# Kernel tuning notes

Hardware: AMD Instinct MI355X
Metric: run time of the kernel (lower is better)

Reference implementation:

```python
import jax, jax.numpy as jnp
import numpy as np

N_NODES = 50000
N_EDGES = 800000
D = 128


def gcn_conv(x, src, dst, W, b, num_nodes):
    # PyG GCNConv: h = X W; add self-loops; symmetric deg^-1/2 normalization; scatter-add; + bias
    h = x @ W                                   # [N, F_out]
    ones = jnp.ones(src.shape[0], dtype=h.dtype)
    deg = jax.ops.segment_sum(ones, dst, num_segments=num_nodes)  # in-degree incl. self-loops
    dinv = jax.lax.rsqrt(jnp.maximum(deg, 1.0))  # deg >= 1 because of self-loops
    norm = dinv[src] * dinv[dst]                 # [E+N]
    msg = h[src] * norm[:, None]                 # gather + scale
    out = jax.ops.segment_sum(msg, dst, num_segments=num_nodes)
    return out + b


def setup_inputs() -> dict:
    key = jax.random.key(0)
    ks = jax.random.split(key, 6)
    x = jax.random.normal(ks[0], (N_NODES, D), dtype=jnp.float32)
    edge_index = jax.random.randint(ks[1], (2, N_EDGES), 0, N_NODES, dtype=jnp.int64)
    s = 1.0 / np.sqrt(D)
    W1 = jax.random.normal(ks[2], (D, D), dtype=jnp.float32) * s
    W2 = jax.random.normal(ks[3], (D, D), dtype=jnp.float32) * s
    Wg = jax.random.normal(ks[4], (2 * D, D), dtype=jnp.float32) * (1.0 / np.sqrt(2 * D))
    b1 = jnp.zeros((D,), jnp.float32)
    b2 = jnp.zeros((D,), jnp.float32)
    bg = jnp.zeros((D,), jnp.float32)
    return {"x": x, "edge_index": edge_index, "W1": W1, "b1": b1,
            "W2": W2, "b2": b2, "Wg": Wg, "bg": bg}


def reference(x, edge_index, W1, b1, W2, b2, Wg, bg):
    num_nodes = x.shape[0]
    x0 = jnp.clip(x, -100.0, 100.0)
    loop = jnp.arange(num_nodes, dtype=edge_index.dtype)
    src = jnp.concatenate([edge_index[0], loop])
    dst = jnp.concatenate([edge_index[1], loop])
    h = jax.nn.relu(gcn_conv(x0, src, dst, W1, b1, num_nodes))
    # F.dropout(p=0.3, training=False) -> identity at inference
    h = jax.nn.relu(gcn_conv(h, src, dst, W2, b2, num_nodes))
    h = h + x0  # residual (out_channels == in_channels)
    gate = jax.nn.sigmoid(jnp.concatenate([h, x0], axis=1) @ Wg + bg)
    return h * gate
```

## Files before the change

### kernel.cpp

```cpp
#include <hip/hip_runtime.h>
#include <hip/hip_bf16.h>

using short8 = __attribute__((ext_vector_type(8))) short;
using f32x4  = __attribute__((ext_vector_type(4))) float;

static constexpr int NN = 50000;
static constexpr int NE = 800000;
static constexpr int MPAD = 50048;
static constexpr int NB2 = 256;
static constexpr int BNODE = 196;
static constexpr int CAPB = 4096;
static constexpr int NCHB = 200;
static constexpr int CHB = NE / NCHB;

__device__ __forceinline__ float clip100(float v) { return fminf(fmaxf(v, -100.f), 100.f); }
__device__ __forceinline__ unsigned short f2b(float v) {
    __hip_bfloat16 h = __float2bfloat16(v);
    return *reinterpret_cast<unsigned short*>(&h);
}
__device__ __forceinline__ float blo(unsigned int u) { return __uint_as_float(u << 16); }
__device__ __forceinline__ float bhi(unsigned int u) { return __uint_as_float(u & 0xFFFF0000u); }
__device__ __forceinline__ float b2f(unsigned short u) {
    return __uint_as_float(((unsigned int)u) << 16);
}

__global__ __launch_bounds__(256) void k_front(const int* __restrict__ idx,
                                               int2* __restrict__ epair,
                                               int* __restrict__ gcur,
                                               const float* __restrict__ W1,
                                               const float* __restrict__ W2,
                                               const float* __restrict__ Wg,
                                               unsigned short* __restrict__ Wt1,
                                               unsigned short* __restrict__ Wt2,
                                               unsigned short* __restrict__ Wgt) {
    __shared__ int ls[CHB], ld[CHB];
    __shared__ int bcnt[NB2], bb[NB2], bofs[NB2];
    const int tid = threadIdx.x;
    if (blockIdx.x < NCHB) {
        const int beg = blockIdx.x * CHB;
        for (int i = tid; i < CHB; i += 256) {
            ls[i] = idx[beg + i];
            ld[i] = idx[NE + beg + i];
        }
        bcnt[tid] = 0;
        __syncthreads();
        for (int i = tid; i < CHB; i += 256) atomicAdd(&bcnt[ld[i] / BNODE], 1);
        __syncthreads();
        bb[tid] = atomicAdd(&gcur[tid], bcnt[tid]);
        bofs[tid] = 0;
        __syncthreads();
        for (int i = tid; i < CHB; i += 256) {
            const int d = ld[i];
            const int p = d / BNODE;
            const int pos = atomicAdd(&bofs[p], 1);
            epair[p * CAPB + bb[p] + pos] = make_int2(ls[i], d);
        }
    } else {
        const int i = (blockIdx.x - NCHB) * 256 + tid;
        if (i < 16384) {
            const int n = i >> 7, k = i & 127;
            Wt1[i] = f2b(W1[k * 128 + n]);
        } else if (i < 32768) {
            const int j = i - 16384;
            const int n = j >> 7, k = j & 127;
            Wt2[j] = f2b(W2[k * 128 + n]);
        } else {
            const int j = i - 32768;
            const int n = j >> 8, k = j & 255;
            Wgt[j] = f2b(Wg[k * 128 + n]);
        }
    }
}

__global__ __launch_bounds__(256) void k_mid(const int2* __restrict__ epair,
                                             const int* __restrict__ gcur,
                                             int* __restrict__ rowptr,
                                             float* __restrict__ dinv,
                                             int* __restrict__ esrc,
                                             const float* __restrict__ x,
                                             const unsigned short* __restrict__ Wt,
                                             unsigned short* __restrict__ Cb) {
    __shared__ alignas(16) char smem[CAPB * 2 * 4 + 3 * 256 * 4];
    const int tid = threadIdx.x;
    if (blockIdx.x < NB2) {
        int* ls   = (int*)smem;
        int* ld   = ls + CAPB;
        int* cntL = ld + CAPB;
        int* sc   = cntL + 256;
        int* cur  = sc + 256;
        const int t = tid;
        const int b = blockIdx.x;
        sc[t] = gcur[t];
        __syncthreads();
        for (int off = 1; off < 256; off <<= 1) {
            const int add = (t >= off) ? sc[t - off] : 0;
            __syncthreads();
            sc[t] += add;
            __syncthreads();
        }
        const int ne = gcur[b];
        const int base = sc[b] - ne;
        const int nb0 = b * BNODE;
        const int nn = min(NN - nb0, BNODE);
        if (b == 0 && t == 0) rowptr[NN] = NE;

        for (int i = t; i < ne; i += 256) {
            const int2 p = epair[b * CAPB + i];
            ls[i] = p.x;
            ld[i] = p.y - nb0;
        }
        cntL[t] = 0;
        __syncthreads();
        for (int i = t; i < ne; i += 256) atomicAdd(&cntL[ld[i]], 1);
        __syncthreads();
        sc[t] = cntL[t];
        __syncthreads();
        for (int off = 1; off < 256; off <<= 1) {
            const int add = (t >= off) ? sc[t - off] : 0;
            __syncthreads();
            sc[t] += add;
            __syncthreads();
        }
        const int excl = sc[t] - cntL[t];
        cur[t] = excl;
        if (t < nn) {
            rowptr[nb0 + t] = base + excl;
            dinv[nb0 + t] = rsqrtf(1.f + (float)cntL[t]);
        }
        __syncthreads();
        for (int i = t; i < ne; i += 256) {
            const int pos = base + atomicAdd(&cur[ld[i]], 1);
            esrc[pos] = ls[i];
        }
    } else {
        unsigned short* wl = (unsigned short*)smem;
#pragma unroll
        for (int j = tid; j < 2048; j += 256) {
            const int row = j >> 4, c8 = j & 15;
            *(short8*)(wl + row * 136 + c8 * 8) = *(const short8*)(Wt + row * 128 + c8 * 8);
        }
        __syncthreads();

        const int wv = tid >> 6;
        const int ln = tid & 63;
        const int l16 = ln & 15;
        const int qd = ln >> 4;
        const int rowb = (blockIdx.x - NB2) * 64 + wv * 16;
        const long arow = rowb + l16;
        const int kq = qd * 8;

        f32x4 acc[8];
#pragma unroll
        for (int i = 0; i < 8; ++i) acc[i] = (f32x4){0.f, 0.f, 0.f, 0.f};

#pragma unroll
        for (int kc = 0; kc < 4; ++kc) {
            short8 a = (short8){0, 0, 0, 0, 0, 0, 0, 0};
            if (arow < NN) {
                const float* fp = x + arow * 128 + kc * 32 + kq;
                const float4 f0 = *(const float4*)fp;
                const float4 f1 = *(const float4*)(fp + 4);
                a[0] = (short)f2b(clip100(f0.x));
                a[1] = (short)f2b(clip100(f0.y));
                a[2] = (short)f2b(clip100(f0.z));
                a[3] = (short)f2b(clip100(f0.w));
                a[4] = (short)f2b(clip100(f1.x));
                a[5] = (short)f2b(clip100(f1.y));
                a[6] = (short)f2b(clip100(f1.z));
                a[7] = (short)f2b(clip100(f1.w));
            }
#pragma unroll
            for (int nt = 0; nt < 8; ++nt) {
                const short8 b = *(const short8*)(wl + (nt * 16 + l16) * 136 + kc * 32 + kq);
                acc[nt] = __builtin_amdgcn_mfma_f32_16x16x32_bf16(a, b, acc[nt], 0, 0, 0);
            }
        }

        const int r0 = rowb + qd * 4;
#pragma unroll
        for (int r = 0; r < 4; ++r) {
            const int row = r0 + r;
            if (row < NN) {
#pragma unroll
                for (int nt = 0; nt < 8; ++nt) {
                    Cb[(long)row * 128 + nt * 16 + l16] = f2b(acc[nt][r]);
                }
            }
        }
    }
}

__global__ __launch_bounds__(256) void k_mfma2(const unsigned short* __restrict__ Ab,
                                               const unsigned short* __restrict__ Wt,
                                               unsigned short* __restrict__ Cb,
                                               const float* __restrict__ dinv) {
    __shared__ unsigned short wl[128 * 136];
    const int tid = threadIdx.x;
#pragma unroll
    for (int j = tid; j < 2048; j += 256) {
        const int row = j >> 4, c8 = j & 15;
        *(short8*)(wl + row * 136 + c8 * 8) = *(const short8*)(Wt + row * 128 + c8 * 8);
    }
    __syncthreads();

    const int wv = tid >> 6;
    const int ln = tid & 63;
    const int l16 = ln & 15;
    const int qd = ln >> 4;
    const int rowb = blockIdx.x * 64 + wv * 16;
    const long arow = rowb + l16;
    const int kq = qd * 8;

    f32x4 acc[8];
#pragma unroll
    for (int i = 0; i < 8; ++i) acc[i] = (f32x4){0.f, 0.f, 0.f, 0.f};

#pragma unroll
    for (int kc = 0; kc < 4; ++kc) {
        const short8 a = *(const short8*)(Ab + arow * 128 + kc * 32 + kq);
#pragma unroll
        for (int nt = 0; nt < 8; ++nt) {
            const short8 b = *(const short8*)(wl + (nt * 16 + l16) * 136 + kc * 32 + kq);
            acc[nt] = __builtin_amdgcn_mfma_f32_16x16x32_bf16(a, b, acc[nt], 0, 0, 0);
        }
    }

    const int r0 = rowb + qd * 4;
#pragma unroll
    for (int r = 0; r < 4; ++r) {
        const int row = r0 + r;
        if (row < NN) {
            const float dv = dinv[row];
#pragma unroll
            for (int nt = 0; nt < 8; ++nt) {
                Cb[(long)row * 128 + nt * 16 + l16] = f2b(acc[nt][r] * dv);
            }
        }
    }
}

__global__ __launch_bounds__(256) void k_mfma_gate(const unsigned short* __restrict__ Ab,
                                                   const float* __restrict__ Af,
                                                   const unsigned short* __restrict__ Wt,
                                                   const float* __restrict__ bg,
                                                   float* __restrict__ out) {
    __shared__ unsigned short wl[128 * 136];
    const int tid = threadIdx.x;
    const int wv = tid >> 6;
    const int ln = tid & 63;
    const int l16 = ln & 15;
    const int qd = ln >> 4;
    const int rowb = blockIdx.x * 64 + wv * 16;
    const long arow = rowb + l16;
    const int kq = qd * 8;

    f32x4 acc[8];
#pragma unroll
    for (int i = 0; i < 8; ++i) acc[i] = (f32x4){0.f, 0.f, 0.f, 0.f};

#pragma unroll
    for (int j = tid; j < 2048; j += 256) {
        const int row = j >> 4, c8 = j & 15;
        *(short8*)(wl + row * 136 + c8 * 8) = *(const short8*)(Wt + row * 256 + c8 * 8);
    }
    __syncthreads();
    {
        const unsigned short* ap = Ab + arow * 128 + kq;
#pragma unroll
        for (int kc = 0; kc < 4; ++kc) {
            const short8 a = *(const short8*)(ap + kc * 32);
#pragma unroll
            for (int nt = 0; nt < 8; ++nt) {
                const short8 b = *(const short8*)(wl + (nt * 16 + l16) * 136 + kc * 32 + kq);
                acc[nt] = __builtin_amdgcn_mfma_f32_16x16x32_bf16(a, b, acc[nt], 0, 0, 0);
            }
        }
    }
    __syncthreads();

#pragma unroll
    for (int j = tid; j < 2048; j += 256) {
        const int row = j >> 4, c8 = j & 15;
        *(short8*)(wl + row * 136 + c8 * 8) = *(const short8*)(Wt + row * 256 + 128 + c8 * 8);
    }
    __syncthreads();
    {
        const bool valid = arow < NN;
        const float* fp = Af + arow * 128 + kq;
#pragma unroll
        for (int kc = 0; kc < 4; ++kc) {
            short8 a = (short8){0, 0, 0, 0, 0, 0, 0, 0};
            if (valid) {
                const float4 f0 = *(const float4*)(fp + kc * 32);
                const float4 f1 = *(const float4*)(fp + kc * 32 + 4);
                a[0] = (short)f2b(clip100(f0.x));
                a[1] = (short)f2b(clip100(f0.y));
                a[2] = (short)f2b(clip100(f0.z));
                a[3] = (short)f2b(clip100(f0.w));
                a[4] = (short)f2b(clip100(f1.x));
                a[5] = (short)f2b(clip100(f1.y));
                a[6] = (short)f2b(clip100(f1.z));
                a[7] = (short)f2b(clip100(f1.w));
            }
#pragma unroll
            for (int nt = 0; nt < 8; ++nt) {
                const short8 b = *(const short8*)(wl + (nt * 16 + l16) * 136 + kc * 32 + kq);
                acc[nt] = __builtin_amdgcn_mfma_f32_16x16x32_bf16(a, b, acc[nt], 0, 0, 0);
            }
        }
    }

    const int r0 = rowb + qd * 4;
#pragma unroll
    for (int nt = 0; nt < 8; ++nt) {
        const int col = nt * 16 + l16;
        const float bgv = bg[col];
#pragma unroll
        for (int r = 0; r < 4; ++r) {
            const int row = r0 + r;
            if (row < NN) {
                const float g = 1.f / (1.f + __expf(-(acc[nt][r] + bgv)));
                const float ov = b2f(Ab[(long)row * 128 + col]) * g;
                __builtin_nontemporal_store(ov, &out[(long)row * 128 + col]);
            }
        }
    }
}

template <bool RES, bool ESCALE>
__global__ __launch_bounds__(256) void k_aggr(const unsigned int* __restrict__ As2,
                                              unsigned short* __restrict__ Bb,
                                              const int* __restrict__ rowptr,
                                              const int* __restrict__ esrc,
                                              const float* __restrict__ dinv,
                                              const float* __restrict__ bias,
                                              const float* __restrict__ x) {
    const int d = __builtin_amdgcn_readfirstlane((blockIdx.x * 256 + threadIdx.x) >> 6);
    if (d >= NN) return;
    const int lane = threadIdx.x & 63;
    const float dd = dinv[d];

    const unsigned int u = As2[(long)d * 64 + lane];
    float2 acc;
    if (ESCALE) {
        acc.x = blo(u) * dd;
        acc.y = bhi(u) * dd;
    } else {
        acc.x = blo(u);
        acc.y = bhi(u);
    }

    const int beg = rowptr[d];
    const int end = rowptr[d + 1];
    int i = beg;
    for (; i + 16 <= end; i += 16) {
        int s[16];
#pragma unroll
        for (int e = 0; e < 16; ++e) s[e] = esrc[i + e];
        unsigned int v[16];
#pragma unroll
        for (int e = 0; e < 16; ++e) v[e] = As2[(long)s[e] * 64 + lane];
        if (ESCALE) {
            float px = 0.f, py = 0.f;
#pragma unroll
            for (int e = 0; e < 16; ++e) {
                const float w = dinv[s[e]];
                px = fmaf(blo(v[e]), w, px);
                py = fmaf(bhi(v[e]), w, py);
            }
            acc.x += px;
            acc.y += py;
        } else {
            float px = 0.f, py = 0.f;
#pragma unroll
            for (int e = 0; e < 16; ++e) {
                px += blo(v[e]);
                py += bhi(v[e]);
            }
            acc.x += px;
            acc.y += py;
        }
    }
    if (i + 8 <= end) {
        const int s0 = esrc[i + 0], s1 = esrc[i + 1], s2 = esrc[i + 2], s3 = esrc[i + 3];
        const int s4 = esrc[i + 4], s5 = esrc[i + 5], s6 = esrc[i + 6], s7 = esrc[i + 7];
        const unsigned int v0 = As2[(long)s0 * 64 + lane];
        const unsigned int v1 = As2[(long)s1 * 64 + lane];
        const unsigned int v2 = As2[(long)s2 * 64 + lane];
        const unsigned int v3 = As2[(long)s3 * 64 + lane];
        const unsigned int v4 = As2[(long)s4 * 64 + lane];
        const unsigned int v5 = As2[(long)s5 * 64 + lane];
        const unsigned int v6 = As2[(long)s6 * 64 + lane];
        const unsigned int v7 = As2[(long)s7 * 64 + lane];
        if (ESCALE) {
            const float w0 = dinv[s0], w1 = dinv[s1], w2 = dinv[s2], w3 = dinv[s3];
            const float w4 = dinv[s4], w5 = dinv[s5], w6 = dinv[s6], w7 = dinv[s7];
            acc.x += ((blo(v0) * w0 + blo(v1) * w1) + (blo(v2) * w2 + blo(v3) * w3)) +
                     ((blo(v4) * w4 + blo(v5) * w5) + (blo(v6) * w6 + blo(v7) * w7));
            acc.y += ((bhi(v0) * w0 + bhi(v1) * w1) + (bhi(v2) * w2 + bhi(v3) * w3)) +
                     ((bhi(v4) * w4 + bhi(v5) * w5) + (bhi(v6) * w6 + bhi(v7) * w7));
        } else {
            acc.x += ((blo(v0) + blo(v1)) + (blo(v2) + blo(v3))) +
                     ((blo(v4) + blo(v5)) + (blo(v6) + blo(v7)));
            acc.y += ((bhi(v0) + bhi(v1)) + (bhi(v2) + bhi(v3))) +
                     ((bhi(v4) + bhi(v5)) + (bhi(v6) + bhi(v7)));
        }
        i += 8;
    }
    if (i + 4 <= end) {
        const int s0 = esrc[i + 0], s1 = esrc[i + 1], s2 = esrc[i + 2], s3 = esrc[i + 3];
        const unsigned int v0 = As2[(long)s0 * 64 + lane];
        const unsigned int v1 = As2[(long)s1 * 64 + lane];
        const unsigned int v2 = As2[(long)s2 * 64 + lane];
        const unsigned int v3 = As2[(long)s3 * 64 + lane];
        if (ESCALE) {
            const float w0 = dinv[s0], w1 = dinv[s1], w2 = dinv[s2], w3 = dinv[s3];
            acc.x += (blo(v0) * w0 + blo(v1) * w1) + (blo(v2) * w2 + blo(v3) * w3);
            acc.y += (bhi(v0) * w0 + bhi(v1) * w1) + (bhi(v2) * w2 + bhi(v3) * w3);
        } else {
            acc.x += (blo(v0) + blo(v1)) + (blo(v2) + blo(v3));
            acc.y += (bhi(v0) + bhi(v1)) + (bhi(v2) + bhi(v3));
        }
        i += 4;
    }
    for (; i < end; ++i) {
        const int s = esrc[i];
        const unsigned int v = As2[(long)s * 64 + lane];
        if (ESCALE) {
            const float w = dinv[s];
            acc.x = fmaf(blo(v), w, acc.x);
            acc.y = fmaf(bhi(v), w, acc.y);
        } else {
            acc.x += blo(v);
            acc.y += bhi(v);
        }
    }

    const float2 bv = ((const float2*)bias)[lane];
    acc.x = fmaxf(fmaf(acc.x, dd, bv.x), 0.f);
    acc.y = fmaxf(fmaf(acc.y, dd, bv.y), 0.f);
    if (RES) {
        const float2 xv = ((const float2*)x)[(long)d * 64 + lane];
        acc.x += clip100(xv.x);
        acc.y += clip100(xv.y);
    }
    const unsigned int pack = (unsigned int)f2b(acc.x) | ((unsigned int)f2b(acc.y) << 16);
    ((unsigned int*)Bb)[(long)d * 64 + lane] = pack;
}

extern "C" void kernel_launch(void* const* d_in, const int* in_sizes, int n_in,
                              void* d_out, int out_size, void* d_ws, size_t ws_size,
                              hipStream_t stream) {
    const float* x  = (const float*)d_in[0];
    const int*  eix = (const int*)d_in[1];
    const float* W1 = (const float*)d_in[2];
    const float* b1 = (const float*)d_in[3];
    const float* W2 = (const float*)d_in[4];
    const float* b2 = (const float*)d_in[5];
    const float* Wg = (const float*)d_in[6];
    const float* bg = (const float*)d_in[7];
    float* out = (float*)d_out;

    char* ws = (char*)d_ws;
    unsigned short* As   = (unsigned short*)ws;
    unsigned short* hb   = (unsigned short*)(ws + 12812288);
    unsigned short* Wt1  = (unsigned short*)(ws + 25624576);
    unsigned short* Wt2  = (unsigned short*)(ws + 25657344);
    unsigned short* Wgt  = (unsigned short*)(ws + 25690112);
    int*   rowptr = (int*)(ws + 25755648);
    float* dinv   = (float*)(ws + 25956352);
    int*   gcur   = (int*)(ws + 26157056);
    int*   esrc   = (int*)(ws + 26159104);
    int2*  epair  = (int2*)(ws + 29359104);

    const int ggrid = MPAD / 64;
    dim3 blk(256);

    hipMemsetAsync(gcur, 0, NB2 * sizeof(int), stream);

    k_front<<<NCHB + 256, blk, 0, stream>>>(eix, epair, gcur, W1, W2, Wg, Wt1, Wt2, Wgt);

    k_mid<<<NB2 + ggrid, blk, 0, stream>>>(epair, gcur, rowptr, dinv, esrc, x, Wt1, As);

    k_aggr<false, true><<<(NN * 64 + 255) / 256, blk, 0, stream>>>(
        (const unsigned int*)As, hb, rowptr, esrc, dinv, b1, nullptr);

    k_mfma2<<<ggrid, blk, 0, stream>>>(hb, Wt2, As, dinv);

    k_aggr<true, false><<<(NN * 64 + 255) / 256, blk, 0, stream>>>(
        (const unsigned int*)As, hb, rowptr, esrc, dinv, b2, x);

    k_mfma_gate<<<ggrid, blk, 0, stream>>>(hb, x, Wgt, bg, out);
}
```

Before: 212.0 us.

## Fuse neighbor aggregation with following MFMA GEMMs via shared-memory tiles

Replaces the separate aggregation kernels and the GEMM kernels with two fused kernels. Each wave aggregates 16 nodes sequentially into a shared-memory bf16 tile, then the block runs the MFMA product against the staged weights. This removes the global round trip of the intermediate hidden features and two launches. The cost is less parallelism in aggregation: one wave now serially handles 16 nodes in a grid of about 782 blocks, where before each node had its own wave, so latency hiding in the gather may suffer.

```diff
diff --git a/kernel.cpp b/kernel.cpp
--- a/kernel.cpp
+++ b/kernel.cpp
@@ -24,322 +24,15 @@
     return __uint_as_float(((unsigned int)u) << 16);
 }
 
-__global__ __launch_bounds__(256) void k_front(const int* __restrict__ idx,
-                                               int2* __restrict__ epair,
-                                               int* __restrict__ gcur,
-                                               const float* __restrict__ W1,
-                                               const float* __restrict__ W2,
-                                               const float* __restrict__ Wg,
-                                               unsigned short* __restrict__ Wt1,
-                                               unsigned short* __restrict__ Wt2,
-                                               unsigned short* __restrict__ Wgt) {
-    __shared__ int ls[CHB], ld[CHB];
-    __shared__ int bcnt[NB2], bb[NB2], bofs[NB2];
-    const int tid = threadIdx.x;
-    if (blockIdx.x < NCHB) {
-        const int beg = blockIdx.x * CHB;
-        for (int i = tid; i < CHB; i += 256) {
-            ls[i] = idx[beg + i];
-            ld[i] = idx[NE + beg + i];
-        }
-        bcnt[tid] = 0;
-        __syncthreads();
-        for (int i = tid; i < CHB; i += 256) atomicAdd(&bcnt[ld[i] / BNODE], 1);
-        __syncthreads();
-        bb[tid] = atomicAdd(&gcur[tid], bcnt[tid]);
-        bofs[tid] = 0;
-        __syncthreads();
-        for (int i = tid; i < CHB; i += 256) {
-            const int d = ld[i];
-            const int p = d / BNODE;
-            const int pos = atomicAdd(&bofs[p], 1);
-            epair[p * CAPB + bb[p] + pos] = make_int2(ls[i], d);
-        }
-    } else {
-        const int i = (blockIdx.x - NCHB) * 256 + tid;
-        if (i < 16384) {
-            const int n = i >> 7, k = i & 127;
-            Wt1[i] = f2b(W1[k * 128 + n]);
-        } else if (i < 32768) {
-            const int j = i - 16384;
-            const int n = j >> 7, k = j & 127;
-            Wt2[j] = f2b(W2[k * 128 + n]);
-        } else {
-            const int j = i - 32768;
-            const int n = j >> 8, k = j & 255;
-            Wgt[j] = f2b(Wg[k * 128 + n]);
-        }
-    }
-}
-
-__global__ __launch_bounds__(256) void k_mid(const int2* __restrict__ epair,
-                                             const int* __restrict__ gcur,
-                                             int* __restrict__ rowptr,
-                                             float* __restrict__ dinv,
-                                             int* __restrict__ esrc,
-                                             const float* __restrict__ x,
-                                             const unsigned short* __restrict__ Wt,
-                                             unsigned short* __restrict__ Cb) {
-    __shared__ alignas(16) char smem[CAPB * 2 * 4 + 3 * 256 * 4];
-    const int tid = threadIdx.x;
-    if (blockIdx.x < NB2) {
-        int* ls   = (int*)smem;
-        int* ld   = ls + CAPB;
-        int* cntL = ld + CAPB;
-        int* sc   = cntL + 256;
-        int* cur  = sc + 256;
-        const int t = tid;
-        const int b = blockIdx.x;
-        sc[t] = gcur[t];
-        __syncthreads();
-        for (int off = 1; off < 256; off <<= 1) {
-            const int add = (t >= off) ? sc[t - off] : 0;
-            __syncthreads();
-            sc[t] += add;
-            __syncthreads();
-        }
-        const int ne = gcur[b];
-        const int base = sc[b] - ne;
-        const int nb0 = b * BNODE;
-        const int nn = min(NN - nb0, BNODE);
-        if (b == 0 && t == 0) rowptr[NN] = NE;
-
-        for (int i = t; i < ne; i += 256) {
-            const int2 p = epair[b * CAPB + i];
-            ls[i] = p.x;
-            ld[i] = p.y - nb0;
-        }
-        cntL[t] = 0;
-        __syncthreads();
-        for (int i = t; i < ne; i += 256) atomicAdd(&cntL[ld[i]], 1);
-        __syncthreads();
-        sc[t] = cntL[t];
-        __syncthreads();
-        for (int off = 1; off < 256; off <<= 1) {
-            const int add = (t >= off) ? sc[t - off] : 0;
-            __syncthreads();
-            sc[t] += add;
-            __syncthreads();
-        }
-        const int excl = sc[t] - cntL[t];
-        cur[t] = excl;
-        if (t < nn) {
-            rowptr[nb0 + t] = base + excl;
-            dinv[nb0 + t] = rsqrtf(1.f + (float)cntL[t]);
-        }
-        __syncthreads();
-        for (int i = t; i < ne; i += 256) {
-            const int pos = base + atomicAdd(&cur[ld[i]], 1);
-            esrc[pos] = ls[i];
-        }
-    } else {
-        unsigned short* wl = (unsigned short*)smem;
-#pragma unroll
-        for (int j = tid; j < 2048; j += 256) {
-            const int row = j >> 4, c8 = j & 15;
-            *(short8*)(wl + row * 136 + c8 * 8) = *(const short8*)(Wt + row * 128 + c8 * 8);
-        }
-        __syncthreads();
-
-        const int wv = tid >> 6;
-        const int ln = tid & 63;
-        const int l16 = ln & 15;
-        const int qd = ln >> 4;
-        const int rowb = (blockIdx.x - NB2) * 64 + wv * 16;
-        const long arow = rowb + l16;
-        const int kq = qd * 8;
-
-        f32x4 acc[8];
-#pragma unroll
-        for (int i = 0; i < 8; ++i) acc[i] = (f32x4){0.f, 0.f, 0.f, 0.f};
-
-#pragma unroll
-        for (int kc = 0; kc < 4; ++kc) {
-            short8 a = (short8){0, 0, 0, 0, 0, 0, 0, 0};
-            if (arow < NN) {
-                const float* fp = x + arow * 128 + kc * 32 + kq;
-                const float4 f0 = *(const float4*)fp;
-                const float4 f1 = *(const float4*)(fp + 4);
-                a[0] = (short)f2b(clip100(f0.x));
-                a[1] = (short)f2b(clip100(f0.y));
-                a[2] = (short)f2b(clip100(f0.z));
-                a[3] = (short)f2b(clip100(f0.w));
-                a[4] = (short)f2b(clip100(f1.x));
-                a[5] = (short)f2b(clip100(f1.y));
-                a[6] = (short)f2b(clip100(f1.z));
-                a[7] = (short)f2b(clip100(f1.w));
-            }
-#pragma unroll
-            for (int nt = 0; nt < 8; ++nt) {
-                const short8 b = *(const short8*)(wl + (nt * 16 + l16) * 136 + kc * 32 + kq);
-                acc[nt] = __builtin_amdgcn_mfma_f32_16x16x32_bf16(a, b, acc[nt], 0, 0, 0);
-            }
-        }
-
-        const int r0 = rowb + qd * 4;
-#pragma unroll
-        for (int r = 0; r < 4; ++r) {
-            const int row = r0 + r;
-            if (row < NN) {
-#pragma unroll
-                for (int nt = 0; nt < 8; ++nt) {
-                    Cb[(long)row * 128 + nt * 16 + l16] = f2b(acc[nt][r]);
-                }
-            }
-        }
-    }
-}
-
-__global__ __launch_bounds__(256) void k_mfma2(const unsigned short* __restrict__ Ab,
-                                               const unsigned short* __restrict__ Wt,
-                                               unsigned short* __restrict__ Cb,
-                                               const float* __restrict__ dinv) {
-    __shared__ unsigned short wl[128 * 136];
-    const int tid = threadIdx.x;
-#pragma unroll
-    for (int j = tid; j < 2048; j += 256) {
-        const int row = j >> 4, c8 = j & 15;
-        *(short8*)(wl + row * 136 + c8 * 8) = *(const short8*)(Wt + row * 128 + c8 * 8);
-    }
-    __syncthreads();
-
-    const int wv = tid >> 6;
-    const int ln = tid & 63;
-    const int l16 = ln & 15;
-    const int qd = ln >> 4;
-    const int rowb = blockIdx.x * 64 + wv * 16;
-    const long arow = rowb + l16;
-    const int kq = qd * 8;
-
-    f32x4 acc[8];
-#pragma unroll
-    for (int i = 0; i < 8; ++i) acc[i] = (f32x4){0.f, 0.f, 0.f, 0.f};
-
-#pragma unroll
-    for (int kc = 0; kc < 4; ++kc) {
-        const short8 a = *(const short8*)(Ab + arow * 128 + kc * 32 + kq);
-#pragma unroll
-        for (int nt = 0; nt < 8; ++nt) {
-            const short8 b = *(const short8*)(wl + (nt * 16 + l16) * 136 + kc * 32 + kq);
-            acc[nt] = __builtin_amdgcn_mfma_f32_16x16x32_bf16(a, b, acc[nt], 0, 0, 0);
-        }
-    }
-
-    const int r0 = rowb + qd * 4;
-#pragma unroll
-    for (int r = 0; r < 4; ++r) {
-        const int row = r0 + r;
-        if (row < NN) {
-            const float dv = dinv[row];
-#pragma unroll
-            for (int nt = 0; nt < 8; ++nt) {
-                Cb[(long)row * 128 + nt * 16 + l16] = f2b(acc[nt][r] * dv);
-            }
-        }
-    }
-}
-
-__global__ __launch_bounds__(256) void k_mfma_gate(const unsigned short* __restrict__ Ab,
-                                                   const float* __restrict__ Af,
-                                                   const unsigned short* __restrict__ Wt,
-                                                   const float* __restrict__ bg,
-                                                   float* __restrict__ out) {
-    __shared__ unsigned short wl[128 * 136];
-    const int tid = threadIdx.x;
-    const int wv = tid >> 6;
-    const int ln = tid & 63;
-    const int l16 = ln & 15;
-    const int qd = ln >> 4;
-    const int rowb = blockIdx.x * 64 + wv * 16;
-    const long arow = rowb + l16;
-    const int kq = qd * 8;
-
-    f32x4 acc[8];
-#pragma unroll
-    for (int i = 0; i < 8; ++i) acc[i] = (f32x4){0.f, 0.f, 0.f, 0.f};
-
-#pragma unroll
-    for (int j = tid; j < 2048; j += 256) {
-        const int row = j >> 4, c8 = j & 15;
-        *(short8*)(wl + row * 136 + c8 * 8) = *(const short8*)(Wt + row * 256 + c8 * 8);
-    }
-    __syncthreads();
-    {
-        const unsigned short* ap = Ab + arow * 128 + kq;
-#pragma unroll
-        for (int kc = 0; kc < 4; ++kc) {
-            const short8 a = *(const short8*)(ap + kc * 32);
-#pragma unroll
-            for (int nt = 0; nt < 8; ++nt) {
-                const short8 b = *(const short8*)(wl + (nt * 16 + l16) * 136 + kc * 32 + kq);
-                acc[nt] = __builtin_amdgcn_mfma_f32_16x16x32_bf16(a, b, acc[nt], 0, 0, 0);
-            }
-        }
-    }
-    __syncthreads();
-
-#pragma unroll
-    for (int j = tid; j < 2048; j += 256) {
-        const int row = j >> 4, c8 = j & 15;
-        *(short8*)(wl + row * 136 + c8 * 8) = *(const short8*)(Wt + row * 256 + 128 + c8 * 8);
-    }
-    __syncthreads();
-    {
-        const bool valid = arow < NN;
-        const float* fp = Af + arow * 128 + kq;
-#pragma unroll
-        for (int kc = 0; kc < 4; ++kc) {
-            short8 a = (short8){0, 0, 0, 0, 0, 0, 0, 0};
-            if (valid) {
-                const float4 f0 = *(const float4*)(fp + kc * 32);
-                const float4 f1 = *(const float4*)(fp + kc * 32 + 4);
-                a[0] = (short)f2b(clip100(f0.x));
-                a[1] = (short)f2b(clip100(f0.y));
-                a[2] = (short)f2b(clip100(f0.z));
-                a[3] = (short)f2b(clip100(f0.w));
-                a[4] = (short)f2b(clip100(f1.x));
-                a[5] = (short)f2b(clip100(f1.y));
-                a[6] = (short)f2b(clip100(f1.z));
-                a[7] = (short)f2b(clip100(f1.w));
-            }
-#pragma unroll
-            for (int nt = 0; nt < 8; ++nt) {
-                const short8 b = *(const short8*)(wl + (nt * 16 + l16) * 136 + kc * 32 + kq);
-                acc[nt] = __builtin_amdgcn_mfma_f32_16x16x32_bf16(a, b, acc[nt], 0, 0, 0);
-            }
-        }
-    }
-
-    const int r0 = rowb + qd * 4;
-#pragma unroll
-    for (int nt = 0; nt < 8; ++nt) {
-        const int col = nt * 16 + l16;
-        const float bgv = bg[col];
-#pragma unroll
-        for (int r = 0; r < 4; ++r) {
-            const int row = r0 + r;
-            if (row < NN) {
-                const float g = 1.f / (1.f + __expf(-(acc[nt][r] + bgv)));
-                const float ov = b2f(Ab[(long)row * 128 + col]) * g;
-                __builtin_nontemporal_store(ov, &out[(long)row * 128 + col]);
-            }
-        }
-    }
-}
-
 template <bool RES, bool ESCALE>
-__global__ __launch_bounds__(256) void k_aggr(const unsigned int* __restrict__ As2,
-                                              unsigned short* __restrict__ Bb,
-                                              const int* __restrict__ rowptr,
-                                              const int* __restrict__ esrc,
-                                              const float* __restrict__ dinv,
-                                              const float* __restrict__ bias,
-                                              const float* __restrict__ x) {
-    const int d = __builtin_amdgcn_readfirstlane((blockIdx.x * 256 + threadIdx.x) >> 6);
-    if (d >= NN) return;
-    const int lane = threadIdx.x & 63;
+__device__ __forceinline__ unsigned int aggr_node(const int d, const int lane,
+                                                  const unsigned int* __restrict__ As2,
+                                                  const int* __restrict__ rowptr,
+                                                  const int* __restrict__ esrc,
+                                                  const float* __restrict__ dinv,
+                                                  const float* __restrict__ bias,
+                                                  const float* __restrict__ x) {
     const float dd = dinv[d];
-
     const unsigned int u = As2[(long)d * 64 + lane];
     float2 acc;
     if (ESCALE) {
@@ -349,7 +42,6 @@
         acc.x = blo(u);
         acc.y = bhi(u);
     }
-
     const int beg = rowptr[d];
     const int end = rowptr[d + 1];
     int i = beg;
@@ -360,26 +52,23 @@
         unsigned int v[16];
 #pragma unroll
         for (int e = 0; e < 16; ++e) v[e] = As2[(long)s[e] * 64 + lane];
+        float px = 0.f, py = 0.f;
         if (ESCALE) {
-            float px = 0.f, py = 0.f;
 #pragma unroll
             for (int e = 0; e < 16; ++e) {
                 const float w = dinv[s[e]];
                 px = fmaf(blo(v[e]), w, px);
                 py = fmaf(bhi(v[e]), w, py);
             }
-            acc.x += px;
-            acc.y += py;
         } else {
-            float px = 0.f, py = 0.f;
 #pragma unroll
             for (int e = 0; e < 16; ++e) {
                 px += blo(v[e]);
                 py += bhi(v[e]);
             }
-            acc.x += px;
-            acc.y += py;
-        }
+        }
+        acc.x += px;
+        acc.y += py;
     }
     if (i + 8 <= end) {
         const int s0 = esrc[i + 0], s1 = esrc[i + 1], s2 = esrc[i + 2], s3 = esrc[i + 3];
@@ -435,7 +124,6 @@
             acc.y += bhi(v);
         }
     }
-
     const float2 bv = ((const float2*)bias)[lane];
     acc.x = fmaxf(fmaf(acc.x, dd, bv.x), 0.f);
     acc.y = fmaxf(fmaf(acc.y, dd, bv.y), 0.f);
@@ -444,8 +132,332 @@
         acc.x += clip100(xv.x);
         acc.y += clip100(xv.y);
     }
-    const unsigned int pack = (unsigned int)f2b(acc.x) | ((unsigned int)f2b(acc.y) << 16);
-    ((unsigned int*)Bb)[(long)d * 64 + lane] = pack;
+    return (unsigned int)f2b(acc.x) | ((unsigned int)f2b(acc.y) << 16);
+}
+
+__global__ __launch_bounds__(256) void k_front(const int* __restrict__ idx,
+                                               int2* __restrict__ epair,
+                                               int* __restrict__ gcur,
+                                               const float* __restrict__ W1,
+                                               const float* __restrict__ W2,
+                                               const float* __restrict__ Wg,
+                                               unsigned short* __restrict__ Wt1,
+                                               unsigned short* __restrict__ Wt2,
+                                               unsigned short* __restrict__ Wgt) {
+    __shared__ int ls[CHB], ld[CHB];
+    __shared__ int bcnt[NB2], bb[NB2], bofs[NB2];
+    const int tid = threadIdx.x;
+    if (blockIdx.x < NCHB) {
+        const int beg = blockIdx.x * CHB;
+        for (int i = tid; i < CHB; i += 256) {
+            ls[i] = idx[beg + i];
+            ld[i] = idx[NE + beg + i];
+        }
+        bcnt[tid] = 0;
+        __syncthreads();
+        for (int i = tid; i < CHB; i += 256) atomicAdd(&bcnt[ld[i] / BNODE], 1);
+        __syncthreads();
+        bb[tid] = atomicAdd(&gcur[tid], bcnt[tid]);
+        bofs[tid] = 0;
+        __syncthreads();
+        for (int i = tid; i < CHB; i += 256) {
+            const int d = ld[i];
+            const int p = d / BNODE;
+            const int pos = atomicAdd(&bofs[p], 1);
+            epair[p * CAPB + bb[p] + pos] = make_int2(ls[i], d);
+        }
+    } else {
+        const int i = (blockIdx.x - NCHB) * 256 + tid;
+        if (i < 16384) {
+            const int n = i >> 7, k = i & 127;
+            Wt1[i] = f2b(W1[k * 128 + n]);
+        } else if (i < 32768) {
+            const int j = i - 16384;
+            const int n = j >> 7, k = j & 127;
+            Wt2[j] = f2b(W2[k * 128 + n]);
+        } else {
+            const int j = i - 32768;
+            const int n = j >> 8, k = j & 255;
+            Wgt[j] = f2b(Wg[k * 128 + n]);
+        }
+    }
+}
+
+__global__ __launch_bounds__(256) void k_mid(const int2* __restrict__ epair,
+                                             const int* __restrict__ gcur,
+                                             int* __restrict__ rowptr,
+                                             float* __restrict__ dinv,
+                                             int* __restrict__ esrc,
+                                             const float* __restrict__ x,
+                                             const unsigned short* __restrict__ Wt,
+                                             unsigned short* __restrict__ Cb) {
+    __shared__ alignas(16) char smem[CAPB * 2 * 4 + 3 * 256 * 4];
+    const int tid = threadIdx.x;
+    if (blockIdx.x < NB2) {
+        int* ls   = (int*)smem;
+        int* ld   = ls + CAPB;
+        int* cntL = ld + CAPB;
+        int* sc   = cntL + 256;
+        int* cur  = sc + 256;
+        const int t = tid;
+        const int b = blockIdx.x;
+        sc[t] = gcur[t];
+        __syncthreads();
+        for (int off = 1; off < 256; off <<= 1) {
+            const int add = (t >= off) ? sc[t - off] : 0;
+            __syncthreads();
+            sc[t] += add;
+            __syncthreads();
+        }
+        const int ne = gcur[b];
+        const int base = sc[b] - ne;
+        const int nb0 = b * BNODE;
+        const int nn = min(NN - nb0, BNODE);
+        if (b == 0 && t == 0) rowptr[NN] = NE;
+
+        for (int i = t; i < ne; i += 256) {
+            const int2 p = epair[b * CAPB + i];
+            ls[i] = p.x;
+            ld[i] = p.y - nb0;
+        }
+        cntL[t] = 0;
+        __syncthreads();
+        for (int i = t; i < ne; i += 256) atomicAdd(&cntL[ld[i]], 1);
+        __syncthreads();
+        sc[t] = cntL[t];
+        __syncthreads();
+        for (int off = 1; off < 256; off <<= 1) {
+            const int add = (t >= off) ? sc[t - off] : 0;
+            __syncthreads();
+            sc[t] += add;
+            __syncthreads();
+        }
+        const int excl = sc[t] - cntL[t];
+        cur[t] = excl;
+        if (t < nn) {
+            rowptr[nb0 + t] = base + excl;
+            dinv[nb0 + t] = rsqrtf(1.f + (float)cntL[t]);
+        }
+        __syncthreads();
+        for (int i = t; i < ne; i += 256) {
+            const int pos = base + atomicAdd(&cur[ld[i]], 1);
+            esrc[pos] = ls[i];
+        }
+    } else {
+        unsigned short* wl = (unsigned short*)smem;
+#pragma unroll
+        for (int j = tid; j < 2048; j += 256) {
+            const int row = j >> 4, c8 = j & 15;
+            *(short8*)(wl + row * 136 + c8 * 8) = *(const short8*)(Wt + row * 128 + c8 * 8);
+        }
+        __syncthreads();
+
+        const int wv = tid >> 6;
+        const int ln = tid & 63;
+        const int l16 = ln & 15;
+        const int qd = ln >> 4;
+        const int rowb = (blockIdx.x - NB2) * 64 + wv * 16;
+        const long arow = rowb + l16;
+        const int kq = qd * 8;
+
+        f32x4 acc[8];
+#pragma unroll
+        for (int i = 0; i < 8; ++i) acc[i] = (f32x4){0.f, 0.f, 0.f, 0.f};
+
+#pragma unroll
+        for (int kc = 0; kc < 4; ++kc) {
+            short8 a = (short8){0, 0, 0, 0, 0, 0, 0, 0};
+            if (arow < NN) {
+                const float* fp = x + arow * 128 + kc * 32 + kq;
+                const float4 f0 = *(const float4*)fp;
+                const float4 f1 = *(const float4*)(fp + 4);
+                a[0] = (short)f2b(clip100(f0.x));
+                a[1] = (short)f2b(clip100(f0.y));
+                a[2] = (short)f2b(clip100(f0.z));
+                a[3] = (short)f2b(clip100(f0.w));
+                a[4] = (short)f2b(clip100(f1.x));
+                a[5] = (short)f2b(clip100(f1.y));
+                a[6] = (short)f2b(clip100(f1.z));
+                a[7] = (short)f2b(clip100(f1.w));
+            }
+#pragma unroll
+            for (int nt = 0; nt < 8; ++nt) {
+                const short8 b = *(const short8*)(wl + (nt * 16 + l16) * 136 + kc * 32 + kq);
+                acc[nt] = __builtin_amdgcn_mfma_f32_16x16x32_bf16(a, b, acc[nt], 0, 0, 0);
+            }
+        }
+
+        const int r0 = rowb + qd * 4;
+#pragma unroll
+        for (int r = 0; r < 4; ++r) {
+            const int row = r0 + r;
+            if (row < NN) {
+#pragma unroll
+                for (int nt = 0; nt < 8; ++nt) {
+                    Cb[(long)row * 128 + nt * 16 + l16] = f2b(acc[nt][r]);
+                }
+            }
+        }
+    }
+}
+
+__global__ __launch_bounds__(256) void k_ag1(const unsigned int* __restrict__ As2,
+                                             const unsigned short* __restrict__ Wt2,
+                                             unsigned short* __restrict__ Cb,
+                                             const int* __restrict__ rowptr,
+                                             const int* __restrict__ esrc,
+                                             const float* __restrict__ dinv,
+                                             const float* __restrict__ b1) {
+    __shared__ alignas(16) unsigned int ht[64 * 68];
+    __shared__ unsigned short wl[128 * 136];
+    const int tid = threadIdx.x;
+#pragma unroll
+    for (int j = tid; j < 2048; j += 256) {
+        const int row = j >> 4, c8 = j & 15;
+        *(short8*)(wl + row * 136 + c8 * 8) = *(const short8*)(Wt2 + row * 128 + c8 * 8);
+    }
+    const int wv = tid >> 6;
+    const int ln = tid & 63;
+    const int nbase = blockIdx.x * 64 + wv * 16;
+#pragma unroll 1
+    for (int j = 0; j < 16; ++j) {
+        const int d = __builtin_amdgcn_readfirstlane(nbase + j);
+        unsigned int pack = 0;
+        if (d < NN)
+            pack = aggr_node<false, true>(d, ln, As2, rowptr, esrc, dinv, b1, nullptr);
+        ht[(wv * 16 + j) * 68 + ln] = pack;
+    }
+    __syncthreads();
+
+    const int l16 = ln & 15;
+    const int qd = ln >> 4;
+    const int kq = qd * 8;
+    f32x4 acc[8];
+#pragma unroll
+    for (int i = 0; i < 8; ++i) acc[i] = (f32x4){0.f, 0.f, 0.f, 0.f};
+#pragma unroll
+    for (int kc = 0; kc < 4; ++kc) {
+        const short8 a =
+            *(const short8*)((const unsigned short*)ht + (wv * 16 + l16) * 136 + kc * 32 + kq);
+#pragma unroll
+        for (int nt = 0; nt < 8; ++nt) {
+            const short8 b = *(const short8*)(wl + (nt * 16 + l16) * 136 + kc * 32 + kq);
+            acc[nt] = __builtin_amdgcn_mfma_f32_16x16x32_bf16(a, b, acc[nt], 0, 0, 0);
+        }
+    }
+    const int r0 = blockIdx.x * 64 + wv * 16 + qd * 4;
+#pragma unroll
+    for (int r = 0; r < 4; ++r) {
+        const int row = r0 + r;
+        if (row < NN) {
+            const float dv = dinv[row];
+#pragma unroll
+            for (int nt = 0; nt < 8; ++nt) {
+                Cb[(long)row * 128 + nt * 16 + l16] = f2b(acc[nt][r] * dv);
+            }
+        }
+    }
+}
+
+__global__ __launch_bounds__(256) void k_ag2(const unsigned int* __restrict__ Hs2,
+                                             const float* __restrict__ x,
+                                             const unsigned short* __restrict__ Wgt,
+                                             const int* __restrict__ rowptr,
+                                             const int* __restrict__ esrc,
+                                             const float* __restrict__ dinv,
+                                             const float* __restrict__ b2,
+                                             const float* __restrict__ bg,
+                                             float* __restrict__ out) {
+    __shared__ alignas(16) unsigned int ht[64 * 68];
+    __shared__ unsigned short wl[128 * 136];
+    const int tid = threadIdx.x;
+#pragma unroll
+    for (int j = tid; j < 2048; j += 256) {
+        const int row = j >> 4, c8 = j & 15;
+        *(short8*)(wl + row * 136 + c8 * 8) = *(const short8*)(Wgt + row * 256 + c8 * 8);
+    }
+    const int wv = tid >> 6;
+    const int ln = tid & 63;
+    const int nbase = blockIdx.x * 64 + wv * 16;
+#pragma unroll 1
+    for (int j = 0; j < 16; ++j) {
+        const int d = __builtin_amdgcn_readfirstlane(nbase + j);
+        unsigned int pack = 0;
+        if (d < NN)
+            pack = aggr_node<true, false>(d, ln, Hs2, rowptr, esrc, dinv, b2, x);
+        ht[(wv * 16 + j) * 68 + ln] = pack;
+    }
+    __syncthreads();
+
+    const int l16 = ln & 15;
+    const int qd = ln >> 4;
+    const int kq = qd * 8;
+    f32x4 acc[8];
+#pragma unroll
+    for (int i = 0; i < 8; ++i) acc[i] = (f32x4){0.f, 0.f, 0.f, 0.f};
+
+#pragma unroll
+    for (int kc = 0; kc < 4; ++kc) {
+        const short8 a =
+            *(const short8*)((const unsigned short*)ht + (wv * 16 + l16) * 136 + kc * 32 + kq);
+#pragma unroll
+        for (int nt = 0; nt < 8; ++nt) {
+            const short8 b = *(const short8*)(wl + (nt * 16 + l16) * 136 + kc * 32 + kq);
+            acc[nt] = __builtin_amdgcn_mfma_f32_16x16x32_bf16(a, b, acc[nt], 0, 0, 0);
+        }
+    }
+    __syncthreads();
+
+#pragma unroll
+    for (int j = tid; j < 2048; j += 256) {
+        const int row = j >> 4, c8 = j & 15;
+        *(short8*)(wl + row * 136 + c8 * 8) = *(const short8*)(Wgt + row * 256 + 128 + c8 * 8);
+    }
+    __syncthreads();
+
+    {
+        const long arow = (long)blockIdx.x * 64 + wv * 16 + l16;
+        const bool valid = arow < NN;
+        const float* fp = x + arow * 128 + kq;
+#pragma unroll
+        for (int kc = 0; kc < 4; ++kc) {
+            short8 a = (short8){0, 0, 0, 0, 0, 0, 0, 0};
+            if (valid) {
+                const float4 f0 = *(const float4*)(fp + kc * 32);
+                const float4 f1 = *(const float4*)(fp + kc * 32 + 4);
+                a[0] = (short)f2b(clip100(f0.x));
+                a[1] = (short)f2b(clip100(f0.y));
+                a[2] = (short)f2b(clip100(f0.z));
+                a[3] = (short)f2b(clip100(f0.w));
+                a[4] = (short)f2b(clip100(f1.x));
+                a[5] = (short)f2b(clip100(f1.y));
+                a[6] = (short)f2b(clip100(f1.z));
+                a[7] = (short)f2b(clip100(f1.w));
+            }
+#pragma unroll
+            for (int nt = 0; nt < 8; ++nt) {
+                const short8 b = *(const short8*)(wl + (nt * 16 + l16) * 136 + kc * 32 + kq);
+                acc[nt] = __builtin_amdgcn_mfma_f32_16x16x32_bf16(a, b, acc[nt], 0, 0, 0);
+            }
+        }
+    }
+
+    const int r0 = blockIdx.x * 64 + wv * 16 + qd * 4;
+#pragma unroll
+    for (int nt = 0; nt < 8; ++nt) {
+        const int col = nt * 16 + l16;
+        const float bgv = bg[col];
+#pragma unroll
+        for (int r = 0; r < 4; ++r) {
+            const int row = r0 + r;
+            if (row < NN) {
+                const float g = 1.f / (1.f + __expf(-(acc[nt][r] + bgv)));
+                const unsigned int hu = ht[(wv * 16 + qd * 4 + r) * 68 + (col >> 1)];
+                const float hv = (col & 1) ? bhi(hu) : blo(hu);
+                __builtin_nontemporal_store(hv * g, &out[(long)row * 128 + col]);
+            }
+        }
+    }
 }
 
 extern "C" void kernel_launch(void* const* d_in, const int* in_sizes, int n_in,
@@ -482,13 +494,9 @@
 
     k_mid<<<NB2 + ggrid, blk, 0, stream>>>(epair, gcur, rowptr, dinv, esrc, x, Wt1, As);
 
-    k_aggr<false, true><<<(NN * 64 + 255) / 256, blk, 0, stream>>>(
-        (const unsigned int*)As, hb, rowptr, esrc, dinv, b1, nullptr);
-
-    k_mfma2<<<ggrid, blk, 0, stream>>>(hb, Wt2, As, dinv);
-
-    k_aggr<true, false><<<(NN * 64 + 255) / 256, blk, 0, stream>>>(
-        (const unsigned int*)As, hb, rowptr, esrc, dinv, b2, x);
-
-    k_mfma_gate<<<ggrid, blk, 0, stream>>>(hb, x, Wgt, bg, out);
-}
+    k_ag1<<<ggrid, blk, 0, stream>>>((const unsigned int*)As, Wt2, hb,
+                                     rowptr, esrc, dinv, b1);
+
+    k_ag2<<<ggrid, blk, 0, stream>>>((const unsigned int*)hb, x, Wgt,
+                                     rowptr, esrc, dinv, b2, bg, out);
+}
```

New measurement: 292.0 us. 37.7% more time.
